# Optimization experiments

Hardware: AMD Instinct MI355X
Metric: run time of the kernel (lower is better)

Reference implementation:

```python
import jax, jax.numpy as jnp
import numpy as np

L = 8          # n_layer
D = 512        # hidden_size
DIN = 1024     # d_inner = 2*D (Mamba expand=2)
DS = 16        # d_state
DTR = 32       # dt_rank = ceil(D/16)
K = 4          # d_conv
NACT = 3       # n_action_to_predict
ADIM = 4
LOSS_COEF = 1.0

def silu(x):
    return x * jax.nn.sigmoid(x)

def rms(x, w, eps=1e-5):
    return x * jax.lax.rsqrt(jnp.mean(x * x, axis=-1, keepdims=True) + eps) * w

def tokenize(images, states, actions, patch_w, patch_b, state_w, state_b, act_w, act_b):
    # images [b,l,3,224,224] -> 14x14 patches of 3*16*16=768 -> mean-pooled image token
    b, l = images.shape[:2]
    p = images.reshape(b, l, 3, 14, 16, 14, 16).transpose(0, 1, 3, 5, 2, 4, 6).reshape(b, l, 196, 768)
    img = jnp.mean(p @ patch_w.T + patch_b, axis=2)            # [b,l,D] token_type 1
    st = states[:, :, 0] @ state_w.T + state_b                 # [b,l,D] token_type 2
    ac = actions[:, :, :NACT - 1] @ act_w.T + act_b            # [b,l,NACT-1,D] token_type 3
    toks = jnp.concatenate([img[:, :, None], st[:, :, None], ac], axis=2)  # [b,l,1+NACT,D]
    return toks.reshape(b, l * (1 + NACT), D)

def mamba_mixer(x, in_w, cw, cb, xpw, dtw, dtb, alog, dp, ow):
    # x: [b,S,D]
    b, S, _ = x.shape
    xz = x @ in_w.T                                   # [b,S,2*DIN]
    xi, z = xz[..., :DIN], xz[..., DIN:]
    # causal depthwise conv, kernel K
    xp = jnp.pad(xi, ((0, 0), (K - 1, 0), (0, 0)))
    xc = cb + sum(cw[:, k] * xp[:, k:k + S, :] for k in range(K))
    xc = silu(xc)
    proj = xc @ xpw.T                                  # [b,S,DTR+2*DS]
    dtr, Bm, Cm = proj[..., :DTR], proj[..., DTR:DTR + DS], proj[..., DTR + DS:]
    dt = jax.nn.softplus(dtr @ dtw.T + dtb)            # [b,S,DIN]
    A = -jnp.exp(alog)                                 # [DIN,DS]
    dA = jnp.exp(dt[..., None] * A)                    # [b,S,DIN,DS]
    dBx = dt[..., None] * Bm[:, :, None, :] * xc[..., None]
    def step(h, inp):
        a_t, bx_t = inp
        h = a_t * h + bx_t
        return h, h
    _, hs = jax.lax.scan(step, jnp.zeros((b, DIN, DS), x.dtype),
                         (dA.swapaxes(0, 1), dBx.swapaxes(0, 1)))  # hs [S,b,DIN,DS]
    y = jnp.einsum('sbdn,bsn->bsd', hs, Cm) + dp * xc
    return (y * silu(z)) @ ow.T

def _forward(images, seq_length, states, actions, action_labels,
             patch_w, patch_b, state_w, state_b, act_w, act_b,
             norm1_w, in_proj_w, conv_w, conv_b, x_proj_w, dt_w, dt_b,
             A_log, Dp, out_proj_w, norm2_w, fc1_w, fc2_w, norm_f_w,
             head_w, head_b):
    b, l = images.shape[:2]
    hidden = tokenize(images, states, actions, patch_w, patch_b, state_w, state_b, act_w, act_b)
    residual = jnp.zeros_like(hidden)
    for i in range(L):
        residual = hidden + residual
        hidden = mamba_mixer(rms(residual, norm1_w[i]), in_proj_w[i], conv_w[i], conv_b[i],
                             x_proj_w[i], dt_w[i], dt_b[i], A_log[i], Dp[i], out_proj_w[i])
        residual = hidden + residual
        g = rms(residual, norm2_w[i]) @ fc1_w[i].T       # GatedMLP fc1 -> [.., 2*DIN]
        hidden = (g[..., :DIN] * silu(g[..., DIN:])) @ fc2_w[i].T
    residual = hidden + residual
    hidden = rms(residual, norm_f_w)
    # static action-token positions: per-frame tokens [img, state, act, act] -> indices 1..3
    hs = hidden.reshape(b, l, 1 + NACT, D)[:, :, 1:, :]
    action_preds = hs @ head_w.T + head_b                # [b,l,NACT,ADIM]
    mask = (jnp.arange(l)[None, :] < seq_length[:, None]).astype(jnp.float32)
    la = jnp.mean(jnp.abs(action_preds - action_labels), axis=(2, 3))
    la = (la * mask).sum(axis=1) / jnp.clip(mask.sum(axis=1), 1.0)
    loss = jnp.mean(la) * LOSS_COEF
    return loss, action_preds

def setup_inputs() -> dict:
    key = jax.random.key(0)
    ks = iter(jax.random.split(key, 40))
    nrm = lambda shape, s=0.02: s * jax.random.normal(next(ks), shape, dtype=jnp.float32)
    inp = {
        'images': jax.random.normal(next(ks), (2, 64, 3, 224, 224), jnp.float32),
        'seq_length': jax.random.randint(next(ks), (2,), 1, 65),
        'states': jax.random.normal(next(ks), (2, 64, NACT, 7), jnp.float32),
        'actions': jax.random.normal(next(ks), (2, 64, NACT, ADIM), jnp.float32),
        'action_labels': jax.random.normal(next(ks), (2, 64, NACT, ADIM), jnp.float32),
        'patch_w': nrm((D, 768)), 'patch_b': jnp.zeros((D,), jnp.float32),
        'state_w': nrm((D, 7)), 'state_b': jnp.zeros((D,), jnp.float32),
        'act_w': nrm((D, ADIM)), 'act_b': jnp.zeros((D,), jnp.float32),
        'norm1_w': jnp.ones((L, D), jnp.float32),
        'in_proj_w': nrm((L, 2 * DIN, D)),
        'conv_w': nrm((L, DIN, K), 0.1), 'conv_b': jnp.zeros((L, DIN), jnp.float32),
        'x_proj_w': nrm((L, DTR + 2 * DS, DIN)),
        'dt_w': nrm((L, DIN, DTR)), 'dt_b': jnp.full((L, DIN), -4.6, jnp.float32),
        'A_log': jnp.log(jnp.broadcast_to(jnp.arange(1, DS + 1, dtype=jnp.float32), (L, DIN, DS))).copy(),
        'Dp': jnp.ones((L, DIN), jnp.float32),
        'out_proj_w': nrm((L, D, DIN)),
        'norm2_w': jnp.ones((L, D), jnp.float32),
        'fc1_w': nrm((L, 2 * DIN, D)), 'fc2_w': nrm((L, D, DIN)),
        'norm_f_w': jnp.ones((D,), jnp.float32),
        'head_w': nrm((ADIM, D)), 'head_b': jnp.zeros((ADIM,), jnp.float32),
    }
    return inp

def reference(images, seq_length, states, actions, action_labels,
              patch_w, patch_b, state_w, state_b, act_w, act_b,
              norm1_w, in_proj_w, conv_w, conv_b, x_proj_w, dt_w, dt_b,
              A_log, Dp, out_proj_w, norm2_w, fc1_w, fc2_w, norm_f_w,
              head_w, head_b):
    return _forward(images, seq_length, states, actions, action_labels,
                    patch_w, patch_b, state_w, state_b, act_w, act_b,
                    norm1_w, in_proj_w, conv_w, conv_b, x_proj_w, dt_w, dt_b,
                    A_log, Dp, out_proj_w, norm2_w, fc1_w, fc2_w, norm_f_w,
                    head_w, head_b)
```

## Files before the change

kernel.cpp:

```cpp
#include <hip/hip_runtime.h>


#define NTOK 512
#define SEQ  256
#define CS   32
#define NC   8

typedef __attribute__((ext_vector_type(8))) short bf16x8;
typedef __attribute__((ext_vector_type(16))) float f32x16;

__device__ __forceinline__ float silu_f(float x) { return x / (1.0f + expf(-x)); }
__device__ __forceinline__ float softplus_f(float x) {
  return (x > 20.0f) ? x : log1pf(expf(x));
}

__device__ __forceinline__ void split_pack(float4 v, uint2* hi, uint2* lo) {
  uint ux = __float_as_uint(v.x), uy = __float_as_uint(v.y);
  uint uz = __float_as_uint(v.z), uw = __float_as_uint(v.w);
  hi->x = (ux >> 16) | (uy & 0xffff0000u);
  hi->y = (uz >> 16) | (uw & 0xffff0000u);
  float lx = v.x - __uint_as_float(ux & 0xffff0000u);
  float ly = v.y - __uint_as_float(uy & 0xffff0000u);
  float lz = v.z - __uint_as_float(uz & 0xffff0000u);
  float lw = v.w - __uint_as_float(uw & 0xffff0000u);
  lo->x = (__float_as_uint(lx) >> 16) | (__float_as_uint(ly) & 0xffff0000u);
  lo->y = (__float_as_uint(lz) >> 16) | (__float_as_uint(lw) & 0xffff0000u);
}

__global__ __launch_bounds__(256) void gemm_bs_k(const float* __restrict__ A,
                                                 const float* __restrict__ B,
                                                 float* __restrict__ C,
                                                 int M, int N, int K, int Kc) {
  __shared__ alignas(16) ushort sAh[2][2][2][512];
  __shared__ alignas(16) ushort sAl[2][2][2][512];
  __shared__ alignas(16) ushort sBh[2][2][2][512];
  __shared__ alignas(16) ushort sBl[2][2][2][512];
  int t = threadIdx.x;
  int bn = blockIdx.x, bm = blockIdx.y, z = blockIdx.z;
  const float* Ab = A + (size_t)bm * 64 * K + (size_t)z * Kc;
  const float* Bb = B + (size_t)bn * 64 * K + (size_t)z * Kc;
  float* Cb = C + (size_t)z * M * N;
  int r = t >> 2, kc = (t & 3) << 2;
  int st = r >> 5, m = r & 31;
  int off = ((kc >> 3) << 8) + (m << 3) + (kc & 7);
  int w = t >> 6, lane = t & 63;
  int wr = w >> 1, wc = w & 1;

  f32x16 acc;
#pragma unroll
  for (int i = 0; i < 16; ++i) acc[i] = 0.f;

  int ns = Kc >> 5;
  const float* Ar = Ab + (size_t)r * K + kc;
  const float* Br = Bb + (size_t)r * K + kc;
  float4 a0 = *(const float4*)&Ar[0];
  float4 a1 = *(const float4*)&Ar[16];
  float4 b0 = *(const float4*)&Br[0];
  float4 b1 = *(const float4*)&Br[16];
  {
    uint2 hi, lo;
    split_pack(a0, &hi, &lo);
    *(uint2*)&sAh[0][0][st][off] = hi; *(uint2*)&sAl[0][0][st][off] = lo;
    split_pack(a1, &hi, &lo);
    *(uint2*)&sAh[0][1][st][off] = hi; *(uint2*)&sAl[0][1][st][off] = lo;
    split_pack(b0, &hi, &lo);
    *(uint2*)&sBh[0][0][st][off] = hi; *(uint2*)&sBl[0][0][st][off] = lo;
    split_pack(b1, &hi, &lo);
    *(uint2*)&sBh[0][1][st][off] = hi; *(uint2*)&sBl[0][1][st][off] = lo;
  }
  __syncthreads();
  for (int ssi = 0; ssi < ns; ++ssi) {
    int buf = ssi & 1;
    if (ssi + 1 < ns) {
      a0 = *(const float4*)&Ar[(ssi + 1) * 32];
      a1 = *(const float4*)&Ar[(ssi + 1) * 32 + 16];
      b0 = *(const float4*)&Br[(ssi + 1) * 32];
      b1 = *(const float4*)&Br[(ssi + 1) * 32 + 16];
    }
    bf16x8 ah = *(bf16x8*)&sAh[buf][0][wr][lane << 3];
    bf16x8 al = *(bf16x8*)&sAl[buf][0][wr][lane << 3];
    bf16x8 bh = *(bf16x8*)&sBh[buf][0][wc][lane << 3];
    bf16x8 bl = *(bf16x8*)&sBl[buf][0][wc][lane << 3];
    acc = __builtin_amdgcn_mfma_f32_32x32x16_bf16(ah, bh, acc, 0, 0, 0);
    acc = __builtin_amdgcn_mfma_f32_32x32x16_bf16(al, bh, acc, 0, 0, 0);
    acc = __builtin_amdgcn_mfma_f32_32x32x16_bf16(ah, bl, acc, 0, 0, 0);
    bf16x8 ah1 = *(bf16x8*)&sAh[buf][1][wr][lane << 3];
    bf16x8 al1 = *(bf16x8*)&sAl[buf][1][wr][lane << 3];
    bf16x8 bh1 = *(bf16x8*)&sBh[buf][1][wc][lane << 3];
    bf16x8 bl1 = *(bf16x8*)&sBl[buf][1][wc][lane << 3];
    acc = __builtin_amdgcn_mfma_f32_32x32x16_bf16(ah1, bh1, acc, 0, 0, 0);
    acc = __builtin_amdgcn_mfma_f32_32x32x16_bf16(al1, bh1, acc, 0, 0, 0);
    acc = __builtin_amdgcn_mfma_f32_32x32x16_bf16(ah1, bl1, acc, 0, 0, 0);
    if (ssi + 1 < ns) {
      uint2 hi, lo;
      split_pack(a0, &hi, &lo);
      *(uint2*)&sAh[buf ^ 1][0][st][off] = hi; *(uint2*)&sAl[buf ^ 1][0][st][off] = lo;
      split_pack(a1, &hi, &lo);
      *(uint2*)&sAh[buf ^ 1][1][st][off] = hi; *(uint2*)&sAl[buf ^ 1][1][st][off] = lo;
      split_pack(b0, &hi, &lo);
      *(uint2*)&sBh[buf ^ 1][0][st][off] = hi; *(uint2*)&sBl[buf ^ 1][0][st][off] = lo;
      split_pack(b1, &hi, &lo);
      *(uint2*)&sBh[buf ^ 1][1][st][off] = hi; *(uint2*)&sBl[buf ^ 1][1][st][off] = lo;
    }
    __syncthreads();
  }
  int col = lane & 31, rq = lane >> 5;
  float* Cw = Cb + (size_t)(bm * 64 + wr * 32) * N + bn * 64 + wc * 32 + col;
#pragma unroll
  for (int rg = 0; rg < 16; ++rg) {
    int row = (rg & 3) + ((rg >> 2) << 3) + (rq << 2);
    Cw[(size_t)row * N] = acc[rg];
  }
}

__global__ __launch_bounds__(256) void gemm_glu_k(const float* __restrict__ G,
                                                  const float* __restrict__ B,
                                                  float* __restrict__ C,
                                                  int M, int N, int K, int Kc) {
  __shared__ alignas(16) ushort sAh[2][2][2][512];
  __shared__ alignas(16) ushort sAl[2][2][2][512];
  __shared__ alignas(16) ushort sBh[2][2][2][512];
  __shared__ alignas(16) ushort sBl[2][2][2][512];
  int t = threadIdx.x;
  int bn = blockIdx.x, bm = blockIdx.y, z = blockIdx.z;
  const float* Gb = G + (size_t)bm * 64 * 2048 + (size_t)z * Kc;
  const float* Bb = B + (size_t)bn * 64 * K + (size_t)z * Kc;
  float* Cb = C + (size_t)z * M * N;
  int r = t >> 2, kc = (t & 3) << 2;
  int st = r >> 5, m = r & 31;
  int off = ((kc >> 3) << 8) + (m << 3) + (kc & 7);
  int w = t >> 6, lane = t & 63;
  int wr = w >> 1, wc = w & 1;

  f32x16 acc;
#pragma unroll
  for (int i = 0; i < 16; ++i) acc[i] = 0.f;

  int ns = Kc >> 5;
  const float* gr = Gb + (size_t)r * 2048 + kc;
  const float* Br = Bb + (size_t)r * K + kc;
  float4 ga0 = *(const float4*)&gr[0];
  float4 gz0 = *(const float4*)&gr[1024];
  float4 ga1 = *(const float4*)&gr[16];
  float4 gz1 = *(const float4*)&gr[1040];
  float4 b0 = *(const float4*)&Br[0];
  float4 b1 = *(const float4*)&Br[16];
  {
    float4 a0 = {ga0.x * silu_f(gz0.x), ga0.y * silu_f(gz0.y),
                 ga0.z * silu_f(gz0.z), ga0.w * silu_f(gz0.w)};
    float4 a1 = {ga1.x * silu_f(gz1.x), ga1.y * silu_f(gz1.y),
                 ga1.z * silu_f(gz1.z), ga1.w * silu_f(gz1.w)};
    uint2 hi, lo;
    split_pack(a0, &hi, &lo);
    *(uint2*)&sAh[0][0][st][off] = hi; *(uint2*)&sAl[0][0][st][off] = lo;
    split_pack(a1, &hi, &lo);
    *(uint2*)&sAh[0][1][st][off] = hi; *(uint2*)&sAl[0][1][st][off] = lo;
    split_pack(b0, &hi, &lo);
    *(uint2*)&sBh[0][0][st][off] = hi; *(uint2*)&sBl[0][0][st][off] = lo;
    split_pack(b1, &hi, &lo);
    *(uint2*)&sBh[0][1][st][off] = hi; *(uint2*)&sBl[0][1][st][off] = lo;
  }
  __syncthreads();
  for (int ssi = 0; ssi < ns; ++ssi) {
    int buf = ssi & 1;
    if (ssi + 1 < ns) {
      ga0 = *(const float4*)&gr[(ssi + 1) * 32];
      gz0 = *(const float4*)&gr[1024 + (ssi + 1) * 32];
      ga1 = *(const float4*)&gr[(ssi + 1) * 32 + 16];
      gz1 = *(const float4*)&gr[1040 + (ssi + 1) * 32];
      b0 = *(const float4*)&Br[(ssi + 1) * 32];
      b1 = *(const float4*)&Br[(ssi + 1) * 32 + 16];
    }
    bf16x8 ah = *(bf16x8*)&sAh[buf][0][wr][lane << 3];
    bf16x8 al = *(bf16x8*)&sAl[buf][0][wr][lane << 3];
    bf16x8 bh = *(bf16x8*)&sBh[buf][0][wc][lane << 3];
    bf16x8 bl = *(bf16x8*)&sBl[buf][0][wc][lane << 3];
    acc = __builtin_amdgcn_mfma_f32_32x32x16_bf16(ah, bh, acc, 0, 0, 0);
    acc = __builtin_amdgcn_mfma_f32_32x32x16_bf16(al, bh, acc, 0, 0, 0);
    acc = __builtin_amdgcn_mfma_f32_32x32x16_bf16(ah, bl, acc, 0, 0, 0);
    bf16x8 ah1 = *(bf16x8*)&sAh[buf][1][wr][lane << 3];
    bf16x8 al1 = *(bf16x8*)&sAl[buf][1][wr][lane << 3];
    bf16x8 bh1 = *(bf16x8*)&sBh[buf][1][wc][lane << 3];
    bf16x8 bl1 = *(bf16x8*)&sBl[buf][1][wc][lane << 3];
    acc = __builtin_amdgcn_mfma_f32_32x32x16_bf16(ah1, bh1, acc, 0, 0, 0);
    acc = __builtin_amdgcn_mfma_f32_32x32x16_bf16(al1, bh1, acc, 0, 0, 0);
    acc = __builtin_amdgcn_mfma_f32_32x32x16_bf16(ah1, bl1, acc, 0, 0, 0);
    if (ssi + 1 < ns) {
      float4 a0 = {ga0.x * silu_f(gz0.x), ga0.y * silu_f(gz0.y),
                   ga0.z * silu_f(gz0.z), ga0.w * silu_f(gz0.w)};
      float4 a1 = {ga1.x * silu_f(gz1.x), ga1.y * silu_f(gz1.y),
                   ga1.z * silu_f(gz1.z), ga1.w * silu_f(gz1.w)};
      uint2 hi, lo;
      split_pack(a0, &hi, &lo);
      *(uint2*)&sAh[buf ^ 1][0][st][off] = hi; *(uint2*)&sAl[buf ^ 1][0][st][off] = lo;
      split_pack(a1, &hi, &lo);
      *(uint2*)&sAh[buf ^ 1][1][st][off] = hi; *(uint2*)&sAl[buf ^ 1][1][st][off] = lo;
      split_pack(b0, &hi, &lo);
      *(uint2*)&sBh[buf ^ 1][0][st][off] = hi; *(uint2*)&sBl[buf ^ 1][0][st][off] = lo;
      split_pack(b1, &hi, &lo);
      *(uint2*)&sBh[buf ^ 1][1][st][off] = hi; *(uint2*)&sBl[buf ^ 1][1][st][off] = lo;
    }
    __syncthreads();
  }
  int col = lane & 31, rq = lane >> 5;
  float* Cw = Cb + (size_t)(bm * 64 + wr * 32) * N + bn * 64 + wc * 32 + col;
#pragma unroll
  for (int rg = 0; rg < 16; ++rg) {
    int row = (rg & 3) + ((rg >> 2) << 3) + (rq << 2);
    Cw[(size_t)row * N] = acc[rg];
  }
}

__global__ void patch_part_k(const float* __restrict__ img, float* __restrict__ pmp) {
  int blk = blockIdx.x;
  int bl = blk / 14, hb = blk % 14;
  int t = threadIdx.x;
  int c = t >> 6, hi = (t >> 2) & 15, wi4 = t & 3;
  const float* base = img + (size_t)bl * 3 * 50176 + (size_t)c * 50176 +
                      (size_t)(hb * 16 + hi) * 224 + wi4 * 4;
  float4 s = {0.f, 0.f, 0.f, 0.f};
#pragma unroll
  for (int wb = 0; wb < 14; ++wb) {
    float4 v = *(const float4*)&base[wb * 16];
    s.x += v.x; s.y += v.y; s.z += v.z; s.w += v.w;
  }
  ((float4*)(pmp + (size_t)blk * 768))[t] = s;
}

__global__ void patch_red_k(const float* __restrict__ pmp, float* __restrict__ meanp) {
  int bl = blockIdx.x;
  int t = threadIdx.x;
  float4 s = {0.f, 0.f, 0.f, 0.f};
  for (int hb = 0; hb < 14; ++hb) {
    float4 v = ((const float4*)(pmp + (size_t)(bl * 14 + hb) * 768))[t];
    s.x += v.x; s.y += v.y; s.z += v.z; s.w += v.w;
  }
  const float inv = 1.0f / 196.0f;
  float4 o = {s.x * inv, s.y * inv, s.z * inv, s.w * inv};
  ((float4*)(meanp + (size_t)bl * 768))[t] = o;
}

__global__ void tokenize_k(const float* __restrict__ imgp,
                           const float* __restrict__ states,
                           const float* __restrict__ actions,
                           const float* __restrict__ pb,
                           const float* __restrict__ sw, const float* __restrict__ sb,
                           const float* __restrict__ aw, const float* __restrict__ ab,
                           float* __restrict__ hidden, float* __restrict__ residual) {
  int tok = blockIdx.x;
  int t = threadIdx.x;
  int j = tok & 3;
  int bl = tok >> 2;
  int o0 = t * 4;
  float out[4];
  if (j == 0) {
    float4 a = ((const float4*)pb)[t];
    const float* ip = imgp + (size_t)bl * 512;
#pragma unroll
    for (int p = 0; p < 8; ++p) {
      float4 v = ((const float4*)(ip + (size_t)p * 65536))[t];
      a.x += v.x; a.y += v.y; a.z += v.z; a.w += v.w;
    }
    out[0] = a.x; out[1] = a.y; out[2] = a.z; out[3] = a.w;
  } else if (j == 1) {
    const float* sv = states + (size_t)bl * 21;
#pragma unroll
    for (int i = 0; i < 4; ++i) {
      int o = o0 + i;
      float acc = sb[o];
      for (int k = 0; k < 7; ++k) acc += sw[o * 7 + k] * sv[k];
      out[i] = acc;
    }
  } else {
    const float* av = actions + ((size_t)bl * 3 + (j - 2)) * 4;
#pragma unroll
    for (int i = 0; i < 4; ++i) {
      int o = o0 + i;
      float acc = ab[o];
      for (int k = 0; k < 4; ++k) acc += aw[o * 4 + k] * av[k];
      out[i] = acc;
    }
  }
  float4 ov = {out[0], out[1], out[2], out[3]};
  ((float4*)(hidden + (size_t)tok * 512))[t] = ov;
  float4 z4 = {0.f, 0.f, 0.f, 0.f};
  ((float4*)(residual + (size_t)tok * 512))[t] = z4;
}

__global__ void addnorm_k(const float* __restrict__ hid, int parts,
                          float* __restrict__ res,
                          const float* __restrict__ w, float* __restrict__ xn) {
  int tok = blockIdx.x;
  int t = threadIdx.x;
  float4* r4 = (float4*)(res + (size_t)tok * 512);
  float4 r = r4[t];
  const float4* hp = (const float4*)(hid + (size_t)tok * 512);
  for (int p = 0; p < parts; ++p) {
    float4 h = hp[t];
    r.x += h.x; r.y += h.y; r.z += h.z; r.w += h.w;
    hp += 65536;
  }
  r4[t] = r;
  float ss = r.x * r.x + r.y * r.y + r.z * r.z + r.w * r.w;
  for (int off = 32; off; off >>= 1) ss += __shfl_down(ss, off, 64);
  __shared__ float s2[2];
  if ((t & 63) == 0) s2[t >> 6] = ss;
  __syncthreads();
  float tot = s2[0] + s2[1];
  float scale = rsqrtf(tot * (1.0f / 512.0f) + 1e-5f);
  float4 wv = ((const float4*)w)[t];
  float4 o = {r.x * scale * wv.x, r.y * scale * wv.y,
              r.z * scale * wv.z, r.w * scale * wv.w};
  ((float4*)(xn + (size_t)tok * 512))[t] = o;
}

__global__ __launch_bounds__(256) void convproj_k(const float* __restrict__ xz,
                                                  const float* __restrict__ cw,
                                                  const float* __restrict__ cb,
                                                  const float* __restrict__ xpw,
                                                  const float* __restrict__ dtw,
                                                  const float* __restrict__ dtbias,
                                                  float* __restrict__ xc,
                                                  float* __restrict__ proj,
                                                  float* __restrict__ dt) {
  int tok = blockIdx.x;
  int t = threadIdx.x;
  int b = tok >> 8, s = tok & 255;
  __shared__ float xr[1024];
  __shared__ float pp[4][64];
  __shared__ float pr[64];
  int d4 = t * 4;
  float4 cw0 = ((const float4*)cw)[d4];
  float4 cw1 = ((const float4*)cw)[d4 + 1];
  float4 cw2 = ((const float4*)cw)[d4 + 2];
  float4 cw3 = ((const float4*)cw)[d4 + 3];
  float acc0 = cb[d4], acc1 = cb[d4 + 1], acc2 = cb[d4 + 2], acc3 = cb[d4 + 3];
  const float* base = xz + (size_t)b * 256 * 2048 + d4;
  const float wk0[4] = {cw0.x, cw0.y, cw0.z, cw0.w};
  const float wk1[4] = {cw1.x, cw1.y, cw1.z, cw1.w};
  const float wk2[4] = {cw2.x, cw2.y, cw2.z, cw2.w};
  const float wk3[4] = {cw3.x, cw3.y, cw3.z, cw3.w};
#pragma unroll
  for (int k = 0; k < 4; ++k) {
    int row = s + k - 3;
    if (row >= 0) {
      float4 v = *(const float4*)&base[(size_t)row * 2048];
      acc0 += wk0[k] * v.x; acc1 += wk1[k] * v.y;
      acc2 += wk2[k] * v.z; acc3 += wk3[k] * v.w;
    }
  }
  float4 xc4 = {silu_f(acc0), silu_f(acc1), silu_f(acc2), silu_f(acc3)};
  ((float4*)(xc + (size_t)tok * 1024))[t] = xc4;
  *(float4*)&xr[d4] = xc4;
  __syncthreads();
  int n = t & 63, q = t >> 6;
  {
    const float* wrow = xpw + (size_t)n * 1024 + q * 256;
    const float* xq = xr + q * 256;
    float acc = 0.f;
    for (int k = 0; k < 256; k += 4)
      acc += wrow[k] * xq[k] + wrow[k + 1] * xq[k + 1] +
             wrow[k + 2] * xq[k + 2] + wrow[k + 3] * xq[k + 3];
    pp[q][n] = acc;
  }
  __syncthreads();
  if (t < 64) {
    float v = pp[0][t] + pp[1][t] + pp[2][t] + pp[3][t];
    pr[t] = v;
    proj[(size_t)tok * 64 + t] = v;
  }
  __syncthreads();
#pragma unroll
  for (int i = 0; i < 4; ++i) {
    int d = t * 4 + i;
    const float* dw = dtw + (size_t)d * 32;
    float a = dtbias[d];
    for (int k = 0; k < 32; ++k) a += dw[k] * pr[k];
    dt[(size_t)tok * 1024 + d] = softplus_f(a);
  }
}

__global__ __launch_bounds__(512) void scan_k(const float* __restrict__ dt,
                                              const float* __restrict__ proj,
                                              const float* __restrict__ xc,
                                              const float* __restrict__ xz,
                                              const float* __restrict__ alog,
                                              const float* __restrict__ Dp,
                                              float* __restrict__ yz) {
  __shared__ float sDt[256][4];
  __shared__ float sXc[256][4];
  __shared__ float sZ[256][4];
  __shared__ float sBC[256][32];
  __shared__ float2 sP[8][4][16];
  __shared__ float sY[256][4];
  int t = threadIdx.x;
  int g = blockIdx.x;
  int b = g >> 8;
  int d0 = (g & 255) << 2;
  int c = t >> 6, dl = (t >> 4) & 3, n = t & 15;
  int d = d0 + dl;
  const float* dtb = dt + (size_t)b * 256 * 1024 + d0;
  const float* xcb = xc + (size_t)b * 256 * 1024 + d0;
  const float* zb  = xz + (size_t)b * 256 * 2048 + 1024 + d0;
  const float* pbp = proj + (size_t)b * 256 * 64 + 32;
  float* yb = yz + (size_t)b * 256 * 1024 + d0;

  if (t < 256) {
    *(float4*)&sDt[t][0] = *(const float4*)&dtb[(size_t)t * 1024];
    *(float4*)&sZ[t][0]  = *(const float4*)&zb[(size_t)t * 2048];
  } else {
    int u = t - 256;
    *(float4*)&sXc[u][0] = *(const float4*)&xcb[(size_t)u * 1024];
  }
#pragma unroll
  for (int i = 0; i < 4; ++i) {
    int idx = i * 512 + t;
    int s = idx >> 3, c4 = (idx & 7) << 2;
    *(float4*)&sBC[s][c4] = *(const float4*)&pbp[(size_t)s * 64 + c4];
  }
  float A = -expf(alog[d * 16 + n]);
  float dp = Dp[d];
  __syncthreads();

  float Ap = 1.f, Bacc = 0.f;
#pragma unroll
  for (int i = 0; i < CS; ++i) {
    int s = (c << 5) + i;
    float dtv = sDt[s][dl];
    float dA = __expf(dtv * A);
    Bacc = dA * Bacc + dtv * sBC[s][n] * sXc[s][dl];
    Ap *= dA;
  }
  sP[c][dl][n] = make_float2(Ap, Bacc);
  __syncthreads();

  float h = 0.f;
  for (int cc = 0; cc < c; ++cc) {
    float2 p = sP[cc][dl][n];
    h = p.x * h + p.y;
  }

#pragma unroll
  for (int i = 0; i < CS; ++i) {
    int s = (c << 5) + i;
    float dtv = sDt[s][dl];
    float xcv = sXc[s][dl];
    float dA = __expf(dtv * A);
    h = dA * h + dtv * sBC[s][n] * xcv;
    float yc = h * sBC[s][16 + n];
    yc += __shfl_xor(yc, 1, 64);
    yc += __shfl_xor(yc, 2, 64);
    yc += __shfl_xor(yc, 4, 64);
    yc += __shfl_xor(yc, 8, 64);
    if (n == 0) sY[s][dl] = (yc + dp * xcv) * silu_f(sZ[s][dl]);
  }
  __syncthreads();
  if (t < 256)
    *(float4*)&yb[(size_t)t * 1024] = *(const float4*)&sY[t][0];
}

__global__ void head_k(const float* __restrict__ hf, const float* __restrict__ hw,
                       const float* __restrict__ hb, const float* __restrict__ labels,
                       float* __restrict__ preds, float* __restrict__ labs) {
  int blk = blockIdx.x;
  int j = blk % 3;
  int l = (blk / 3) % 64;
  int b = blk / 192;
  int row = b * 256 + l * 4 + 1 + j;
  int t = threadIdx.x;
  const float* x = hf + (size_t)row * 512;
  float acc[4] = {0.f, 0.f, 0.f, 0.f};
  for (int k = t; k < 512; k += 64) {
    float xv = x[k];
#pragma unroll
    for (int a = 0; a < 4; ++a) acc[a] += xv * hw[a * 512 + k];
  }
  for (int off = 32; off; off >>= 1) {
#pragma unroll
    for (int a = 0; a < 4; ++a) acc[a] += __shfl_down(acc[a], off, 64);
  }
  if (t == 0) {
    const float* lab = labels + (size_t)blk * 4;
    float sd = 0.f;
#pragma unroll
    for (int a = 0; a < 4; ++a) {
      float p = acc[a] + hb[a];
      preds[(size_t)blk * 4 + a] = p;
      sd += fabsf(p - lab[a]);
    }
    labs[blk] = sd;
  }
}

__global__ void loss_k(const float* __restrict__ labs, const int* __restrict__ seqlen,
                       float* __restrict__ out) {
  int t = threadIdx.x;
  int b = t >> 6, l = t & 63;
  float la = (labs[(b * 64 + l) * 3] + labs[(b * 64 + l) * 3 + 1] +
              labs[(b * 64 + l) * 3 + 2]) * (1.0f / 12.0f);
  float m = (l < seqlen[b]) ? 1.f : 0.f;
  float v = la * m;
  for (int off = 32; off; off >>= 1) {
    v += __shfl_down(v, off, 64);
    m += __shfl_down(m, off, 64);
  }
  __shared__ float sb_[2];
  if ((t & 63) == 0) sb_[b] = v / fmaxf(m, 1.0f);
  __syncthreads();
  if (t == 0) out[0] = 0.5f * (sb_[0] + sb_[1]);
}

extern "C" void kernel_launch(void* const* d_in, const int* in_sizes, int n_in,
                              void* d_out, int out_size, void* d_ws, size_t ws_size,
                              hipStream_t stream) {
  const float* images     = (const float*)d_in[0];
  const int*   seq_length = (const int*)d_in[1];
  const float* states     = (const float*)d_in[2];
  const float* actions    = (const float*)d_in[3];
  const float* labels     = (const float*)d_in[4];
  const float* patch_w    = (const float*)d_in[5];
  const float* patch_b    = (const float*)d_in[6];
  const float* state_w    = (const float*)d_in[7];
  const float* state_b    = (const float*)d_in[8];
  const float* act_w      = (const float*)d_in[9];
  const float* act_b      = (const float*)d_in[10];
  const float* norm1_w    = (const float*)d_in[11];
  const float* in_proj_w  = (const float*)d_in[12];
  const float* conv_w     = (const float*)d_in[13];
  const float* conv_b     = (const float*)d_in[14];
  const float* x_proj_w   = (const float*)d_in[15];
  const float* dt_w       = (const float*)d_in[16];
  const float* dt_b       = (const float*)d_in[17];
  const float* A_log      = (const float*)d_in[18];
  const float* Dp         = (const float*)d_in[19];
  const float* out_proj_w = (const float*)d_in[20];
  const float* norm2_w    = (const float*)d_in[21];
  const float* fc1_w      = (const float*)d_in[22];
  const float* fc2_w      = (const float*)d_in[23];
  const float* norm_f_w   = (const float*)d_in[24];
  const float* head_w     = (const float*)d_in[25];
  const float* head_b     = (const float*)d_in[26];

  float* out = (float*)d_out;

  float* ws = (float*)d_ws;
  float* meanp    = ws; ws += 98304;
  float* hidden   = ws; ws += 262144;
  float* residual = ws; ws += 262144;
  float* xn       = ws; ws += 262144;
  float* xz       = ws; ws += 1048576;
  float* xc       = ws; ws += 524288;
  float* proj     = ws; ws += 32768;
  float* dtbuf    = ws; ws += 524288;
  float* yz       = ws; ws += 524288;
  float* labs     = ws; ws += 384;
  float* cpart    = ws; ws += 1048576;
  float* pmp      = ws; ws += 1376256;

  hipLaunchKernelGGL(patch_part_k, dim3(1792), dim3(192), 0, stream, images, pmp);
  hipLaunchKernelGGL(patch_red_k, dim3(128), dim3(192), 0, stream, pmp, meanp);
  hipLaunchKernelGGL(gemm_bs_k, dim3(8, 2, 8), dim3(256), 0, stream,
                     meanp, patch_w, cpart, 128, 512, 768, 96);
  hipLaunchKernelGGL(tokenize_k, dim3(512), dim3(128), 0, stream, cpart, states, actions,
                     patch_b, state_w, state_b, act_w, act_b, hidden, residual);

  for (int i = 0; i < 8; ++i) {
    const float* n1 = norm1_w + i * 512;
    const float* ipw = in_proj_w + (size_t)i * 2048 * 512;
    const float* cw = conv_w + (size_t)i * 4096;
    const float* cb = conv_b + (size_t)i * 1024;
    const float* xpw = x_proj_w + (size_t)i * 65536;
    const float* dtw = dt_w + (size_t)i * 32768;
    const float* dtbias = dt_b + (size_t)i * 1024;
    const float* al = A_log + (size_t)i * 16384;
    const float* dpp = Dp + (size_t)i * 1024;
    const float* opw = out_proj_w + (size_t)i * 524288;
    const float* n2 = norm2_w + i * 512;
    const float* f1 = fc1_w + (size_t)i * 1048576;
    const float* f2 = fc2_w + (size_t)i * 524288;

    if (i == 0)
      hipLaunchKernelGGL(addnorm_k, dim3(512), dim3(128), 0, stream,
                         hidden, 1, residual, n1, xn);
    else
      hipLaunchKernelGGL(addnorm_k, dim3(512), dim3(128), 0, stream,
                         cpart, 4, residual, n1, xn);
    hipLaunchKernelGGL(gemm_bs_k, dim3(32, 8, 1), dim3(256), 0, stream,
                       xn, ipw, xz, 512, 2048, 512, 512);
    hipLaunchKernelGGL(convproj_k, dim3(512), dim3(256), 0, stream,
                       xz, cw, cb, xpw, dtw, dtbias, xc, proj, dtbuf);
    hipLaunchKernelGGL(scan_k, dim3(512), dim3(512), 0, stream,
                       dtbuf, proj, xc, xz, al, dpp, yz);
    hipLaunchKernelGGL(gemm_bs_k, dim3(8, 8, 4), dim3(256), 0, stream,
                       yz, opw, cpart, 512, 512, 1024, 256);
    hipLaunchKernelGGL(addnorm_k, dim3(512), dim3(128), 0, stream,
                       cpart, 4, residual, n2, xn);
    hipLaunchKernelGGL(gemm_bs_k, dim3(32, 8, 1), dim3(256), 0, stream,
                       xn, f1, xz, 512, 2048, 512, 512);
    hipLaunchKernelGGL(gemm_glu_k, dim3(8, 8, 4), dim3(256), 0, stream,
                       xz, f2, cpart, 512, 512, 1024, 256);
  }

  hipLaunchKernelGGL(addnorm_k, dim3(512), dim3(128), 0, stream,
                     cpart, 4, residual, norm_f_w, xn);
  hipLaunchKernelGGL(head_k, dim3(384), dim3(64), 0, stream, xn, head_w, head_b, labels,
                     out + 1, labs);
  hipLaunchKernelGGL(loss_k, dim3(1), dim3(128), 0, stream, labs, seq_length, out);
}
```

Measured before the change: 1.117 ms.

## Split GEMM K across two wave groups, vectorize x_proj, fuse final norm into head

The split-bf16 GEMM kernels now run 512 threads, with two groups of four waves each taking half of every 32-wide K slice. The two partial accumulators are combined through shared memory before the store. This is meant to raise MFMA parallelism and hide load latency per block, at the cost of an extra LDS reduction, more shared memory and higher register pressure under the 512 launch bound. Separately, the x_proj dot product uses float4 loads, and the final add+RMSNorm is fused into the head kernel so only the needed rows are normalized and one launch is dropped.

```diff
diff --git a/kernel.cpp b/kernel.cpp
--- a/kernel.cpp
+++ b/kernel.cpp
@@ -4,7 +4,6 @@
 #define NTOK 512
 #define SEQ  256
 #define CS   32
-#define NC   8
 
 typedef __attribute__((ext_vector_type(8))) short bf16x8;
 typedef __attribute__((ext_vector_type(16))) float f32x16;
@@ -27,24 +26,27 @@
   lo->y = (__float_as_uint(lz) >> 16) | (__float_as_uint(lw) & 0xffff0000u);
 }
 
-__global__ __launch_bounds__(256) void gemm_bs_k(const float* __restrict__ A,
-                                                 const float* __restrict__ B,
-                                                 float* __restrict__ C,
-                                                 int M, int N, int K, int Kc) {
+__global__ __launch_bounds__(512, 2) void gemm_bs_k(const float* __restrict__ A,
+                                                    const float* __restrict__ B,
+                                                    float* __restrict__ C,
+                                                    int M, int N, int K, int Kc) {
   __shared__ alignas(16) ushort sAh[2][2][2][512];
   __shared__ alignas(16) ushort sAl[2][2][2][512];
   __shared__ alignas(16) ushort sBh[2][2][2][512];
   __shared__ alignas(16) ushort sBl[2][2][2][512];
+  __shared__ alignas(64) float sRed[4096];
   int t = threadIdx.x;
   int bn = blockIdx.x, bm = blockIdx.y, z = blockIdx.z;
   const float* Ab = A + (size_t)bm * 64 * K + (size_t)z * Kc;
   const float* Bb = B + (size_t)bn * 64 * K + (size_t)z * Kc;
   float* Cb = C + (size_t)z * M * N;
-  int r = t >> 2, kc = (t & 3) << 2;
+  int r = t >> 3, kc = (t & 7) << 2;
+  int kh = kc >> 4, kc16 = kc & 15;
   int st = r >> 5, m = r & 31;
-  int off = ((kc >> 3) << 8) + (m << 3) + (kc & 7);
+  int off = ((kc16 >> 3) << 8) + (m << 3) + (kc16 & 7);
   int w = t >> 6, lane = t & 63;
-  int wr = w >> 1, wc = w & 1;
+  int g = w >> 2, wq = w & 3;
+  int wr = wq >> 1, wc = wq & 1;
 
   f32x16 acc;
 #pragma unroll
@@ -53,161 +55,132 @@
   int ns = Kc >> 5;
   const float* Ar = Ab + (size_t)r * K + kc;
   const float* Br = Bb + (size_t)r * K + kc;
-  float4 a0 = *(const float4*)&Ar[0];
-  float4 a1 = *(const float4*)&Ar[16];
-  float4 b0 = *(const float4*)&Br[0];
-  float4 b1 = *(const float4*)&Br[16];
+  float4 a4 = *(const float4*)&Ar[0];
+  float4 b4 = *(const float4*)&Br[0];
   {
     uint2 hi, lo;
-    split_pack(a0, &hi, &lo);
-    *(uint2*)&sAh[0][0][st][off] = hi; *(uint2*)&sAl[0][0][st][off] = lo;
-    split_pack(a1, &hi, &lo);
-    *(uint2*)&sAh[0][1][st][off] = hi; *(uint2*)&sAl[0][1][st][off] = lo;
-    split_pack(b0, &hi, &lo);
-    *(uint2*)&sBh[0][0][st][off] = hi; *(uint2*)&sBl[0][0][st][off] = lo;
-    split_pack(b1, &hi, &lo);
-    *(uint2*)&sBh[0][1][st][off] = hi; *(uint2*)&sBl[0][1][st][off] = lo;
+    split_pack(a4, &hi, &lo);
+    *(uint2*)&sAh[0][kh][st][off] = hi; *(uint2*)&sAl[0][kh][st][off] = lo;
+    split_pack(b4, &hi, &lo);
+    *(uint2*)&sBh[0][kh][st][off] = hi; *(uint2*)&sBl[0][kh][st][off] = lo;
   }
   __syncthreads();
   for (int ssi = 0; ssi < ns; ++ssi) {
     int buf = ssi & 1;
     if (ssi + 1 < ns) {
-      a0 = *(const float4*)&Ar[(ssi + 1) * 32];
-      a1 = *(const float4*)&Ar[(ssi + 1) * 32 + 16];
-      b0 = *(const float4*)&Br[(ssi + 1) * 32];
-      b1 = *(const float4*)&Br[(ssi + 1) * 32 + 16];
-    }
-    bf16x8 ah = *(bf16x8*)&sAh[buf][0][wr][lane << 3];
-    bf16x8 al = *(bf16x8*)&sAl[buf][0][wr][lane << 3];
-    bf16x8 bh = *(bf16x8*)&sBh[buf][0][wc][lane << 3];
-    bf16x8 bl = *(bf16x8*)&sBl[buf][0][wc][lane << 3];
+      a4 = *(const float4*)&Ar[(ssi + 1) * 32];
+      b4 = *(const float4*)&Br[(ssi + 1) * 32];
+    }
+    bf16x8 ah = *(bf16x8*)&sAh[buf][g][wr][lane << 3];
+    bf16x8 al = *(bf16x8*)&sAl[buf][g][wr][lane << 3];
+    bf16x8 bh = *(bf16x8*)&sBh[buf][g][wc][lane << 3];
+    bf16x8 bl = *(bf16x8*)&sBl[buf][g][wc][lane << 3];
     acc = __builtin_amdgcn_mfma_f32_32x32x16_bf16(ah, bh, acc, 0, 0, 0);
     acc = __builtin_amdgcn_mfma_f32_32x32x16_bf16(al, bh, acc, 0, 0, 0);
     acc = __builtin_amdgcn_mfma_f32_32x32x16_bf16(ah, bl, acc, 0, 0, 0);
-    bf16x8 ah1 = *(bf16x8*)&sAh[buf][1][wr][lane << 3];
-    bf16x8 al1 = *(bf16x8*)&sAl[buf][1][wr][lane << 3];
-    bf16x8 bh1 = *(bf16x8*)&sBh[buf][1][wc][lane << 3];
-    bf16x8 bl1 = *(bf16x8*)&sBl[buf][1][wc][lane << 3];
-    acc = __builtin_amdgcn_mfma_f32_32x32x16_bf16(ah1, bh1, acc, 0, 0, 0);
-    acc = __builtin_amdgcn_mfma_f32_32x32x16_bf16(al1, bh1, acc, 0, 0, 0);
-    acc = __builtin_amdgcn_mfma_f32_32x32x16_bf16(ah1, bl1, acc, 0, 0, 0);
     if (ssi + 1 < ns) {
       uint2 hi, lo;
-      split_pack(a0, &hi, &lo);
-      *(uint2*)&sAh[buf ^ 1][0][st][off] = hi; *(uint2*)&sAl[buf ^ 1][0][st][off] = lo;
-      split_pack(a1, &hi, &lo);
-      *(uint2*)&sAh[buf ^ 1][1][st][off] = hi; *(uint2*)&sAl[buf ^ 1][1][st][off] = lo;
-      split_pack(b0, &hi, &lo);
-      *(uint2*)&sBh[buf ^ 1][0][st][off] = hi; *(uint2*)&sBl[buf ^ 1][0][st][off] = lo;
-      split_pack(b1, &hi, &lo);
-      *(uint2*)&sBh[buf ^ 1][1][st][off] = hi; *(uint2*)&sBl[buf ^ 1][1][st][off] = lo;
+      split_pack(a4, &hi, &lo);
+      *(uint2*)&sAh[buf ^ 1][kh][st][off] = hi; *(uint2*)&sAl[buf ^ 1][kh][st][off] = lo;
+      split_pack(b4, &hi, &lo);
+      *(uint2*)&sBh[buf ^ 1][kh][st][off] = hi; *(uint2*)&sBl[buf ^ 1][kh][st][off] = lo;
     }
     __syncthreads();
   }
-  int col = lane & 31, rq = lane >> 5;
-  float* Cw = Cb + (size_t)(bm * 64 + wr * 32) * N + bn * 64 + wc * 32 + col;
-#pragma unroll
-  for (int rg = 0; rg < 16; ++rg) {
-    int row = (rg & 3) + ((rg >> 2) << 3) + (rq << 2);
-    Cw[(size_t)row * N] = acc[rg];
-  }
-}
-
-__global__ __launch_bounds__(256) void gemm_glu_k(const float* __restrict__ G,
-                                                  const float* __restrict__ B,
-                                                  float* __restrict__ C,
-                                                  int M, int N, int K, int Kc) {
+  if (g == 1) *(f32x16*)&sRed[(wq * 64 + lane) << 4] = acc;
+  __syncthreads();
+  if (g == 0) {
+    f32x16 o = *(f32x16*)&sRed[(wq * 64 + lane) << 4];
+#pragma unroll
+    for (int i = 0; i < 16; ++i) acc[i] += o[i];
+    int col = lane & 31, rq = lane >> 5;
+    float* Cw = Cb + (size_t)(bm * 64 + wr * 32) * N + bn * 64 + wc * 32 + col;
+#pragma unroll
+    for (int rg = 0; rg < 16; ++rg) {
+      int row = (rg & 3) + ((rg >> 2) << 3) + (rq << 2);
+      Cw[(size_t)row * N] = acc[rg];
+    }
+  }
+}
+
+__global__ __launch_bounds__(512, 2) void gemm_glu_k(const float* __restrict__ G,
+                                                     const float* __restrict__ B,
+                                                     float* __restrict__ C,
+                                                     int M, int N, int K, int Kc) {
   __shared__ alignas(16) ushort sAh[2][2][2][512];
   __shared__ alignas(16) ushort sAl[2][2][2][512];
   __shared__ alignas(16) ushort sBh[2][2][2][512];
   __shared__ alignas(16) ushort sBl[2][2][2][512];
+  __shared__ alignas(64) float sRed[4096];
   int t = threadIdx.x;
   int bn = blockIdx.x, bm = blockIdx.y, z = blockIdx.z;
-  const float* Gb = G + (size_t)bm * 64 * 2048 + (size_t)z * Kc;
-  const float* Bb = B + (size_t)bn * 64 * K + (size_t)z * Kc;
   float* Cb = C + (size_t)z * M * N;
-  int r = t >> 2, kc = (t & 3) << 2;
+  int r = t >> 3, kc = (t & 7) << 2;
+  int kh = kc >> 4, kc16 = kc & 15;
   int st = r >> 5, m = r & 31;
-  int off = ((kc >> 3) << 8) + (m << 3) + (kc & 7);
+  int off = ((kc16 >> 3) << 8) + (m << 3) + (kc16 & 7);
   int w = t >> 6, lane = t & 63;
-  int wr = w >> 1, wc = w & 1;
+  int g = w >> 2, wq = w & 3;
+  int wr = wq >> 1, wc = wq & 1;
 
   f32x16 acc;
 #pragma unroll
   for (int i = 0; i < 16; ++i) acc[i] = 0.f;
 
   int ns = Kc >> 5;
-  const float* gr = Gb + (size_t)r * 2048 + kc;
-  const float* Br = Bb + (size_t)r * K + kc;
-  float4 ga0 = *(const float4*)&gr[0];
-  float4 gz0 = *(const float4*)&gr[1024];
-  float4 ga1 = *(const float4*)&gr[16];
-  float4 gz1 = *(const float4*)&gr[1040];
-  float4 b0 = *(const float4*)&Br[0];
-  float4 b1 = *(const float4*)&Br[16];
+  const float* gr = G + (size_t)(bm * 64 + r) * 2048 + (size_t)z * Kc + kc;
+  const float* Br = B + (size_t)(bn * 64 + r) * K + (size_t)z * Kc + kc;
+  float4 ga = *(const float4*)&gr[0];
+  float4 gz = *(const float4*)&gr[1024];
+  float4 b4 = *(const float4*)&Br[0];
   {
-    float4 a0 = {ga0.x * silu_f(gz0.x), ga0.y * silu_f(gz0.y),
-                 ga0.z * silu_f(gz0.z), ga0.w * silu_f(gz0.w)};
-    float4 a1 = {ga1.x * silu_f(gz1.x), ga1.y * silu_f(gz1.y),
-                 ga1.z * silu_f(gz1.z), ga1.w * silu_f(gz1.w)};
+    float4 a4 = {ga.x * silu_f(gz.x), ga.y * silu_f(gz.y),
+                 ga.z * silu_f(gz.z), ga.w * silu_f(gz.w)};
     uint2 hi, lo;
-    split_pack(a0, &hi, &lo);
-    *(uint2*)&sAh[0][0][st][off] = hi; *(uint2*)&sAl[0][0][st][off] = lo;
-    split_pack(a1, &hi, &lo);
-    *(uint2*)&sAh[0][1][st][off] = hi; *(uint2*)&sAl[0][1][st][off] = lo;
-    split_pack(b0, &hi, &lo);
-    *(uint2*)&sBh[0][0][st][off] = hi; *(uint2*)&sBl[0][0][st][off] = lo;
-    split_pack(b1, &hi, &lo);
-    *(uint2*)&sBh[0][1][st][off] = hi; *(uint2*)&sBl[0][1][st][off] = lo;
+    split_pack(a4, &hi, &lo);
+    *(uint2*)&sAh[0][kh][st][off] = hi; *(uint2*)&sAl[0][kh][st][off] = lo;
+    split_pack(b4, &hi, &lo);
+    *(uint2*)&sBh[0][kh][st][off] = hi; *(uint2*)&sBl[0][kh][st][off] = lo;
   }
   __syncthreads();
   for (int ssi = 0; ssi < ns; ++ssi) {
     int buf = ssi & 1;
     if (ssi + 1 < ns) {
-      ga0 = *(const float4*)&gr[(ssi + 1) * 32];
-      gz0 = *(const float4*)&gr[1024 + (ssi + 1) * 32];
-      ga1 = *(const float4*)&gr[(ssi + 1) * 32 + 16];
-      gz1 = *(const float4*)&gr[1040 + (ssi + 1) * 32];
-      b0 = *(const float4*)&Br[(ssi + 1) * 32];
-      b1 = *(const float4*)&Br[(ssi + 1) * 32 + 16];
-    }
-    bf16x8 ah = *(bf16x8*)&sAh[buf][0][wr][lane << 3];
-    bf16x8 al = *(bf16x8*)&sAl[buf][0][wr][lane << 3];
-    bf16x8 bh = *(bf16x8*)&sBh[buf][0][wc][lane << 3];
-    bf16x8 bl = *(bf16x8*)&sBl[buf][0][wc][lane << 3];
+      ga = *(const float4*)&gr[(ssi + 1) * 32];
+      gz = *(const float4*)&gr[1024 + (ssi + 1) * 32];
+      b4 = *(const float4*)&Br[(ssi + 1) * 32];
+    }
+    bf16x8 ah = *(bf16x8*)&sAh[buf][g][wr][lane << 3];
+    bf16x8 al = *(bf16x8*)&sAl[buf][g][wr][lane << 3];
+    bf16x8 bh = *(bf16x8*)&sBh[buf][g][wc][lane << 3];
+    bf16x8 bl = *(bf16x8*)&sBl[buf][g][wc][lane << 3];
     acc = __builtin_amdgcn_mfma_f32_32x32x16_bf16(ah, bh, acc, 0, 0, 0);
     acc = __builtin_amdgcn_mfma_f32_32x32x16_bf16(al, bh, acc, 0, 0, 0);
     acc = __builtin_amdgcn_mfma_f32_32x32x16_bf16(ah, bl, acc, 0, 0, 0);
-    bf16x8 ah1 = *(bf16x8*)&sAh[buf][1][wr][lane << 3];
-    bf16x8 al1 = *(bf16x8*)&sAl[buf][1][wr][lane << 3];
-    bf16x8 bh1 = *(bf16x8*)&sBh[buf][1][wc][lane << 3];
-    bf16x8 bl1 = *(bf16x8*)&sBl[buf][1][wc][lane << 3];
-    acc = __builtin_amdgcn_mfma_f32_32x32x16_bf16(ah1, bh1, acc, 0, 0, 0);
-    acc = __builtin_amdgcn_mfma_f32_32x32x16_bf16(al1, bh1, acc, 0, 0, 0);
-    acc = __builtin_amdgcn_mfma_f32_32x32x16_bf16(ah1, bl1, acc, 0, 0, 0);
     if (ssi + 1 < ns) {
-      float4 a0 = {ga0.x * silu_f(gz0.x), ga0.y * silu_f(gz0.y),
-                   ga0.z * silu_f(gz0.z), ga0.w * silu_f(gz0.w)};
-      float4 a1 = {ga1.x * silu_f(gz1.x), ga1.y * silu_f(gz1.y),
-                   ga1.z * silu_f(gz1.z), ga1.w * silu_f(gz1.w)};
+      float4 a4 = {ga.x * silu_f(gz.x), ga.y * silu_f(gz.y),
+                   ga.z * silu_f(gz.z), ga.w * silu_f(gz.w)};
       uint2 hi, lo;
-      split_pack(a0, &hi, &lo);
-      *(uint2*)&sAh[buf ^ 1][0][st][off] = hi; *(uint2*)&sAl[buf ^ 1][0][st][off] = lo;
-      split_pack(a1, &hi, &lo);
-      *(uint2*)&sAh[buf ^ 1][1][st][off] = hi; *(uint2*)&sAl[buf ^ 1][1][st][off] = lo;
-      split_pack(b0, &hi, &lo);
-      *(uint2*)&sBh[buf ^ 1][0][st][off] = hi; *(uint2*)&sBl[buf ^ 1][0][st][off] = lo;
-      split_pack(b1, &hi, &lo);
-      *(uint2*)&sBh[buf ^ 1][1][st][off] = hi; *(uint2*)&sBl[buf ^ 1][1][st][off] = lo;
+      split_pack(a4, &hi, &lo);
+      *(uint2*)&sAh[buf ^ 1][kh][st][off] = hi; *(uint2*)&sAl[buf ^ 1][kh][st][off] = lo;
+      split_pack(b4, &hi, &lo);
+      *(uint2*)&sBh[buf ^ 1][kh][st][off] = hi; *(uint2*)&sBl[buf ^ 1][kh][st][off] = lo;
     }
     __syncthreads();
   }
-  int col = lane & 31, rq = lane >> 5;
-  float* Cw = Cb + (size_t)(bm * 64 + wr * 32) * N + bn * 64 + wc * 32 + col;
-#pragma unroll
-  for (int rg = 0; rg < 16; ++rg) {
-    int row = (rg & 3) + ((rg >> 2) << 3) + (rq << 2);
-    Cw[(size_t)row * N] = acc[rg];
+  if (g == 1) *(f32x16*)&sRed[(wq * 64 + lane) << 4] = acc;
+  __syncthreads();
+  if (g == 0) {
+    f32x16 o = *(f32x16*)&sRed[(wq * 64 + lane) << 4];
+#pragma unroll
+    for (int i = 0; i < 16; ++i) acc[i] += o[i];
+    int col = lane & 31, rq = lane >> 5;
+    float* Cw = Cb + (size_t)(bm * 64 + wr * 32) * N + bn * 64 + wc * 32 + col;
+#pragma unroll
+    for (int rg = 0; rg < 16; ++rg) {
+      int row = (rg & 3) + ((rg >> 2) << 3) + (rq << 2);
+      Cw[(size_t)row * N] = acc[rg];
+    }
   }
 }
 
@@ -355,12 +328,15 @@
   __syncthreads();
   int n = t & 63, q = t >> 6;
   {
-    const float* wrow = xpw + (size_t)n * 1024 + q * 256;
-    const float* xq = xr + q * 256;
+    const float4* wrow4 = (const float4*)(xpw + (size_t)n * 1024 + q * 256);
+    const float4* xq4 = (const float4*)(xr + q * 256);
     float acc = 0.f;
-    for (int k = 0; k < 256; k += 4)
-      acc += wrow[k] * xq[k] + wrow[k + 1] * xq[k + 1] +
-             wrow[k + 2] * xq[k + 2] + wrow[k + 3] * xq[k + 3];
+#pragma unroll 8
+    for (int k = 0; k < 64; ++k) {
+      float4 wv = wrow4[k];
+      float4 xv = xq4[k];
+      acc += wv.x * xv.x + wv.y * xv.y + wv.z * xv.z + wv.w * xv.w;
+    }
     pp[q][n] = acc;
   }
   __syncthreads();
@@ -459,8 +435,10 @@
     *(float4*)&yb[(size_t)t * 1024] = *(const float4*)&sY[t][0];
 }
 
-__global__ void head_k(const float* __restrict__ hf, const float* __restrict__ hw,
-                       const float* __restrict__ hb, const float* __restrict__ labels,
+__global__ void head_k(const float* __restrict__ res, const float* __restrict__ part,
+                       const float* __restrict__ wf,
+                       const float* __restrict__ hw, const float* __restrict__ hb,
+                       const float* __restrict__ labels,
                        float* __restrict__ preds, float* __restrict__ labs) {
   int blk = blockIdx.x;
   int j = blk % 3;
@@ -468,12 +446,34 @@
   int b = blk / 192;
   int row = b * 256 + l * 4 + 1 + j;
   int t = threadIdx.x;
-  const float* x = hf + (size_t)row * 512;
+  const float* x = res + (size_t)row * 512;
+  float4 v0 = ((const float4*)x)[t * 2];
+  float4 v1 = ((const float4*)x)[t * 2 + 1];
+#pragma unroll
+  for (int p = 0; p < 4; ++p) {
+    const float* cp = part + (size_t)p * 262144 + (size_t)row * 512;
+    float4 h0 = ((const float4*)cp)[t * 2];
+    float4 h1 = ((const float4*)cp)[t * 2 + 1];
+    v0.x += h0.x; v0.y += h0.y; v0.z += h0.z; v0.w += h0.w;
+    v1.x += h1.x; v1.y += h1.y; v1.z += h1.z; v1.w += h1.w;
+  }
+  float ss = v0.x * v0.x + v0.y * v0.y + v0.z * v0.z + v0.w * v0.w +
+             v1.x * v1.x + v1.y * v1.y + v1.z * v1.z + v1.w * v1.w;
+  for (int off = 32; off; off >>= 1) ss += __shfl_down(ss, off, 64);
+  ss = __shfl(ss, 0, 64);
+  float scale = rsqrtf(ss * (1.0f / 512.0f) + 1e-5f);
+  float4 w0 = ((const float4*)wf)[t * 2];
+  float4 w1 = ((const float4*)wf)[t * 2 + 1];
+  float xn[8] = {v0.x * scale * w0.x, v0.y * scale * w0.y,
+                 v0.z * scale * w0.z, v0.w * scale * w0.w,
+                 v1.x * scale * w1.x, v1.y * scale * w1.y,
+                 v1.z * scale * w1.z, v1.w * scale * w1.w};
   float acc[4] = {0.f, 0.f, 0.f, 0.f};
-  for (int k = t; k < 512; k += 64) {
-    float xv = x[k];
-#pragma unroll
-    for (int a = 0; a < 4; ++a) acc[a] += xv * hw[a * 512 + k];
+#pragma unroll
+  for (int a = 0; a < 4; ++a) {
+    const float* hr = hw + (size_t)a * 512 + t * 8;
+#pragma unroll
+    for (int i = 0; i < 8; ++i) acc[a] += xn[i] * hr[i];
   }
   for (int off = 32; off; off >>= 1) {
 #pragma unroll
@@ -559,7 +559,7 @@
 
   hipLaunchKernelGGL(patch_part_k, dim3(1792), dim3(192), 0, stream, images, pmp);
   hipLaunchKernelGGL(patch_red_k, dim3(128), dim3(192), 0, stream, pmp, meanp);
-  hipLaunchKernelGGL(gemm_bs_k, dim3(8, 2, 8), dim3(256), 0, stream,
+  hipLaunchKernelGGL(gemm_bs_k, dim3(8, 2, 8), dim3(512), 0, stream,
                      meanp, patch_w, cpart, 128, 512, 768, 96);
   hipLaunchKernelGGL(tokenize_k, dim3(512), dim3(128), 0, stream, cpart, states, actions,
                      patch_b, state_w, state_b, act_w, act_b, hidden, residual);
@@ -585,25 +585,23 @@
     else
       hipLaunchKernelGGL(addnorm_k, dim3(512), dim3(128), 0, stream,
                          cpart, 4, residual, n1, xn);
-    hipLaunchKernelGGL(gemm_bs_k, dim3(32, 8, 1), dim3(256), 0, stream,
+    hipLaunchKernelGGL(gemm_bs_k, dim3(32, 8, 1), dim3(512), 0, stream,
                        xn, ipw, xz, 512, 2048, 512, 512);
     hipLaunchKernelGGL(convproj_k, dim3(512), dim3(256), 0, stream,
                        xz, cw, cb, xpw, dtw, dtbias, xc, proj, dtbuf);
     hipLaunchKernelGGL(scan_k, dim3(512), dim3(512), 0, stream,
                        dtbuf, proj, xc, xz, al, dpp, yz);
-    hipLaunchKernelGGL(gemm_bs_k, dim3(8, 8, 4), dim3(256), 0, stream,
+    hipLaunchKernelGGL(gemm_bs_k, dim3(8, 8, 4), dim3(512), 0, stream,
                        yz, opw, cpart, 512, 512, 1024, 256);
     hipLaunchKernelGGL(addnorm_k, dim3(512), dim3(128), 0, stream,
                        cpart, 4, residual, n2, xn);
-    hipLaunchKernelGGL(gemm_bs_k, dim3(32, 8, 1), dim3(256), 0, stream,
+    hipLaunchKernelGGL(gemm_bs_k, dim3(32, 8, 1), dim3(512), 0, stream,
                        xn, f1, xz, 512, 2048, 512, 512);
-    hipLaunchKernelGGL(gemm_glu_k, dim3(8, 8, 4), dim3(256), 0, stream,
+    hipLaunchKernelGGL(gemm_glu_k, dim3(8, 8, 4), dim3(512), 0, stream,
                        xz, f2, cpart, 512, 512, 1024, 256);
   }
 
-  hipLaunchKernelGGL(addnorm_k, dim3(512), dim3(128), 0, stream,
-                     cpart, 4, residual, norm_f_w, xn);
-  hipLaunchKernelGGL(head_k, dim3(384), dim3(64), 0, stream, xn, head_w, head_b, labels,
-                     out + 1, labs);
+  hipLaunchKernelGGL(head_k, dim3(384), dim3(64), 0, stream, residual, cpart,
+                     norm_f_w, head_w, head_b, labels, out + 1, labs);
   hipLaunchKernelGGL(loss_k, dim3(1), dim3(128), 0, stream, labs, seq_length, out);
 }
```

After: 1.129 ms. No clear change (+1.1%).
